# Kernel optimization log

Hardware: AMD Instinct MI355X
Metric: run time of the kernel (lower is better)

## Reference

```python
import jax, jax.numpy as jnp
import numpy as np

# Qwen3-MoE style config
B, S, D = 2, 2048, 2048        # batch, seqlen, hidden_size
E, I, TOPK = 64, 768, 8        # num_experts, moe_intermediate_size, num_experts_per_tok
M = B * S                      # tokens
CAP = 2 * (M * TOPK) // E


def setup_inputs() -> dict:
    key = jax.random.key(0)
    k0, k1, k2, k3, k4 = jax.random.split(key, 5)
    return {
        "x": jax.random.normal(k0, (B, S, D), jnp.float32),
        "router_weight": jax.random.normal(k1, (D, E), jnp.float32) * 0.02,
        "gate_proj": jax.random.normal(k2, (E, D, I), jnp.float32) * 0.02,
        "up_proj": jax.random.normal(k3, (E, D, I), jnp.float32) * 0.02,
        "down_proj": jax.random.normal(k4, (E, I, D), jnp.float32) * 0.02,
    }


def _moe(x, router_weight, gate_proj, up_proj, down_proj):
    b, s, d = x.shape
    xf = x.reshape(-1, d)                                  # [M, d]
    m = xf.shape[0]

    # ---- TokenChoiceTopKRouter: softmax scores, top-k, renormalize ----
    logits = xf @ router_weight                            # [M, E]
    probs = jax.nn.softmax(logits.astype(jnp.float32), axis=-1)
    topw, topi = jax.lax.top_k(probs, TOPK)                # [M, k]
    topw = topw / topw.sum(axis=-1, keepdims=True)         # norm_topk_prob

    flat_e = topi.reshape(-1)                              # [M*k] expert id per assignment
    flat_w = topw.reshape(-1).astype(x.dtype)              # [M*k] routing weight per assignment

    # ---- permute: sort assignments by expert (stable) ----
    order = jnp.argsort(flat_e)                            # [M*k]
    se = flat_e[order]                                     # sorted expert ids
    tok = order // TOPK                                    # source token per sorted assignment
    counts = jax.ops.segment_sum(jnp.ones_like(flat_e), flat_e, num_segments=E)
    starts = jnp.cumsum(counts) - counts                   # exclusive prefix sum
    pos = jnp.arange(m * TOPK) - starts[se]                # slot within expert's buffer
    valid = pos < CAP
    posc = jnp.minimum(pos, CAP - 1)

    # ---- dispatch to padded per-expert buffers [E, CAP, d] ----
    xe = jnp.zeros((E, CAP, d), x.dtype).at[se, pos].set(xf[tok], mode='drop')

    # ---- grouped SwiGLU experts (batched GEMMs) ----
    h = jax.nn.silu(jnp.einsum('ecd,edi->eci', xe, gate_proj)) \
        * jnp.einsum('ecd,edi->eci', xe, up_proj)          # [E, CAP, I]
    ye = jnp.einsum('eci,eid->ecd', h, down_proj)          # [E, CAP, d]

    # ---- unpermute + weighted combine ----
    contrib = jnp.where(valid[:, None], ye[se, posc], 0.0) * flat_w[order][:, None]
    out = jnp.zeros((m, d), x.dtype).at[tok].add(contrib)  # sum over topk per token
    return out.reshape(b, s, d)


def reference(x, router_weight, gate_proj, up_proj, down_proj):
    return _moe(x, router_weight, gate_proj, up_proj, down_proj)
```

## Files before the change

kernel.cpp:

```cpp
#include <hip/hip_runtime.h>
#include <hip/hip_bf16.h>

typedef __attribute__((ext_vector_type(4))) float f32x4;
typedef __attribute__((ext_vector_type(8))) short bf16x8;
typedef __attribute__((ext_vector_type(8))) unsigned short us8;
typedef unsigned int   u32;
typedef unsigned short u16;

#define D_DIM 2048
#define I_DIM 768
#define NE    64
#define CAP   1024
#define NTOK  4096

__device__ __forceinline__ u32 cvt2(float a, float b) {
  __hip_bfloat162 hh = __float22bfloat162_rn(float2{a, b});
  union { __hip_bfloat162 h; u32 u; } c; c.h = hh; return c.u;
}
__device__ __forceinline__ u16 f2b(float f) {
  __hip_bfloat16 b = __float2bfloat16(f);
  union { __hip_bfloat16 b; u16 u; } c; c.b = b; return c.u;
}
__device__ __forceinline__ float b2f(u16 v) {
  union { u32 u; float f; } c; c.u = (u32)v << 16; return c.f;
}
__device__ __forceinline__ void glp16(const void* g, void* l) {
  __builtin_amdgcn_global_load_lds(
      (const __attribute__((address_space(1))) u32*)g,
      (__attribute__((address_space(3))) u32*)l, 16, 0, 0);
}

#define VMW(n) asm volatile("s_waitcnt vmcnt(" #n ")" ::: "memory")
#define BARF   do { __builtin_amdgcn_s_barrier(); \
                    asm volatile("" ::: "memory"); } while (0)

__global__ __launch_bounds__(256) void k_router(
    const float* __restrict__ x, const float* __restrict__ rw,
    int* __restrict__ counts, int* __restrict__ slot_token,
    float* __restrict__ slot_w, u16* __restrict__ xb)
{
  const int lane = threadIdx.x & 63;
  const int tok  = blockIdx.x * 4 + (threadIdx.x >> 6);
  const float* xr = x + (size_t)tok * D_DIM;
  u16* xbr = xb + (size_t)tok * D_DIM;

  float acc = 0.f;
  for (int d0 = 0; d0 < D_DIM; d0 += 64) {
    float xv = xr[d0 + lane];
    xbr[d0 + lane] = f2b(xv);
    #pragma unroll
    for (int j = 0; j < 64; ++j) {
      float xj = __shfl(xv, j, 64);
      acc = fmaf(xj, rw[(size_t)(d0 + j) * NE + lane], acc);
    }
  }

  float v = acc; int vi = lane;
  float wk[8]; int ei[8];
  float mx0 = 0.f, wsum = 0.f;
  #pragma unroll
  for (int k = 0; k < 8; ++k) {
    float mv = v; int mi = vi;
    #pragma unroll
    for (int off = 32; off >= 1; off >>= 1) {
      float ov = __shfl_xor(mv, off, 64);
      int   oi = __shfl_xor(mi, off, 64);
      if (ov > mv || (ov == mv && oi < mi)) { mv = ov; mi = oi; }
    }
    if (k == 0) mx0 = mv;
    float ew = __expf(mv - mx0);
    wk[k] = ew; ei[k] = mi; wsum += ew;
    if (lane == mi) v = -3.4e38f;
  }

  if (lane == 0) {
    float inv = 1.f / wsum;
    #pragma unroll
    for (int k = 0; k < 8; ++k) {
      int ee   = ei[k];
      int slot = atomicAdd(&counts[ee], 1);
      if (slot < CAP) {
        slot_token[ee * CAP + slot] = tok;
        slot_w[ee * CAP + slot]     = wk[k] * inv;
      }
    }
  }
}

__global__ __launch_bounds__(256) void k_inv(
    const int* __restrict__ counts, const int* __restrict__ slot_token,
    int* __restrict__ tok_cnt, int* __restrict__ tok_idx)
{
  const int e = blockIdx.x;
  int cnt = counts[e]; if (cnt > CAP) cnt = CAP;
  for (int s = threadIdx.x; s < cnt; s += 256) {
    const int tok = slot_token[e * CAP + s];
    const int pos = atomicAdd(&tok_cnt[tok], 1);
    if (pos < 8) tok_idx[tok * 8 + pos] = e * CAP + s;
  }
}

__device__ __forceinline__ void wpack_body(const float* __restrict__ ip,
                                           u16* __restrict__ op, int R, int C,
                                           int c0, int r0) {
  __shared__ u16 T[64][76];
  const int t  = threadIdx.x;
  const int rr = t >> 4;
  const int cc = (t & 15) * 4;
  #pragma unroll
  for (int it = 0; it < 4; ++it) {
    const int r = rr + it * 16;
    float4 v = *(const float4*)(ip + (size_t)(r0 + r) * C + c0 + cc);
    T[cc + 0][r] = f2b(v.x);
    T[cc + 1][r] = f2b(v.y);
    T[cc + 2][r] = f2b(v.z);
    T[cc + 3][r] = f2b(v.w);
  }
  __syncthreads();
  const int n = t & 63;
  #pragma unroll
  for (int p = 0; p < 2; ++p) {
    const int c = (t >> 6) + p * 4;
    const u16* s = &T[n][c * 8];
    uint4 o;
    o.x = (u32)s[0] | ((u32)s[1] << 16);
    o.y = (u32)s[2] | ((u32)s[3] << 16);
    o.z = (u32)s[4] | ((u32)s[5] << 16);
    o.w = (u32)s[6] | ((u32)s[7] << 16);
    *(uint4*)(op + ((size_t)c * 64 + n) * 8) = o;
  }
}

__global__ __launch_bounds__(256) void k_wpack_gu(
    const float* __restrict__ g, const float* __restrict__ u,
    u16* __restrict__ og, u16* __restrict__ ou) {
  const int z  = blockIdx.z;
  const int e  = z >> 1;
  const float* in = (z & 1) ? u : g;
  u16* outp       = (z & 1) ? ou : og;
  const int c0 = blockIdx.x * 64;
  const int r0 = blockIdx.y * 64;
  const float* ip = in + (size_t)e * D_DIM * I_DIM;
  u16* op = outp + (size_t)e * (size_t)(I_DIM / 64) * (D_DIM / 8) * 512
                 + ((size_t)(c0 / 64) * (D_DIM / 8) + (r0 / 8)) * 512;
  wpack_body(ip, op, D_DIM, I_DIM, c0, r0);
}

__global__ __launch_bounds__(256) void k_wpack(const float* __restrict__ in,
                                               u16* __restrict__ outp,
                                               int R, int C) {
  const int e  = blockIdx.z;
  const int c0 = blockIdx.x * 64;
  const int r0 = blockIdx.y * 64;
  const float* ip = in + (size_t)e * R * C;
  u16* op = outp + (size_t)e * (size_t)(C / 64) * (R / 8) * 512
                 + ((size_t)(c0 / 64) * (R / 8) + (r0 / 8)) * 512;
  wpack_body(ip, op, R, C, c0, r0);
}

__global__ __launch_bounds__(256) void k_xpack(
    const u16* __restrict__ xb, const int* __restrict__ counts,
    const int* __restrict__ slot_token, u16* __restrict__ xeT)
{
  const int e   = blockIdx.z;
  const int s0  = blockIdx.y * 64;
  const int kc0 = blockIdx.x * 32;
  int cnt = counts[e]; if (cnt > CAP) cnt = CAP;
  const int lim = (cnt + 127) & ~127;
  if (s0 >= lim) return;

  __shared__ u16 T[64][264];
  const int t = threadIdx.x;
  const int r = t >> 2;
  const int q = t & 3;
  const int  tok  = slot_token[e * CAP + s0 + r];
  const bool live = (s0 + r) < cnt;
  const u16* src = xb + (size_t)tok * D_DIM + kc0 * 8;

  #pragma unroll
  for (int it = 0; it < 8; ++it) {
    const int kl = it * 32 + q * 8;
    us8 v = {0, 0, 0, 0, 0, 0, 0, 0};
    if (live) v = *(const us8*)(src + kl);
    *(us8*)&T[r][kl] = v;
  }
  __syncthreads();

  u16* dst = xeT + (size_t)e * 2097152 + (size_t)kc0 * 8192 + (size_t)s0 * 8;
  const int sl = t & 63;
  #pragma unroll
  for (int p = 0; p < 8; ++p) {
    const int c = (t >> 6) + p * 4;
    const u16* s = &T[sl][c * 8];
    uint4 o = *(const uint4*)s;
    *(uint4*)(dst + (size_t)c * 8192 + sl * 8) = o;
  }
}


__device__ __forceinline__ void m1_issue(
    const u16* xeA, const u16* gb, const u16* ub, u16* st,
    int js, int wv, int lane, int m0)
{
  #pragma unroll
  for (int q = 0; q < 6; ++q) {
    const int id = wv * 6 + q;
    const int kc = (id >> 1) & 3;
    const int h  = id & 1;
    const size_t kcA = (size_t)(js * 4 + kc);
    if (id < 8) {
      glp16(xeA + kcA * 8192 + (size_t)(m0 + h * 64 + lane) * 8,
            st + kc * 1024 + h * 512);
    } else if (id < 16) {
      glp16(gb + (size_t)h * 131072 + kcA * 512 + lane * 8,
            st + 4096 + kc * 1024 + h * 512);
    } else {
      glp16(ub + (size_t)h * 131072 + kcA * 512 + lane * 8,
            st + 8192 + kc * 1024 + h * 512);
    }
  }
}

__device__ __forceinline__ void m1_step(
    const u16* st, int gq, int li, int mrow, int icol,
    f32x4 (&ag)[4][4], f32x4 (&au)[4][4])
{
  bf16x8 a[4], g[4], u[4];
  #pragma unroll
  for (int mf = 0; mf < 4; ++mf)
    a[mf] = *(const bf16x8*)&st[(gq * 128 + mrow + mf * 16 + li) * 8];
  #pragma unroll
  for (int nf = 0; nf < 4; ++nf) {
    g[nf] = *(const bf16x8*)&st[4096 + (gq * 128 + icol + nf * 16 + li) * 8];
    u[nf] = *(const bf16x8*)&st[8192 + (gq * 128 + icol + nf * 16 + li) * 8];
  }
  #pragma unroll
  for (int mf = 0; mf < 4; ++mf)
    #pragma unroll
    for (int nf = 0; nf < 4; ++nf) {
      ag[mf][nf] = __builtin_amdgcn_mfma_f32_16x16x32_bf16(a[mf], g[nf], ag[mf][nf], 0, 0, 0);
      au[mf][nf] = __builtin_amdgcn_mfma_f32_16x16x32_bf16(a[mf], u[nf], au[mf][nf], 0, 0, 0);
    }
}

__global__ __launch_bounds__(256, 2) void k_mlp1p(
    const u16* __restrict__ xeT, const u16* __restrict__ Gpk,
    const u16* __restrict__ Upk, const int* __restrict__ counts,
    u16* __restrict__ hP)
{
  extern __shared__ u16 sm[];
  const int i   = blockIdx.x;
  const int xcd = i & 7;
  const int p   = i >> 3;
  const int mt  = p & 7;
  const int pe  = p >> 3;
  const int val = pe * 8 + xcd;
  const int e   = val / 6;
  const int nt  = val % 6;

  int cnt = counts[e]; if (cnt > CAP) cnt = CAP;
  const int m0 = mt * 128;
  if (m0 >= cnt) return;

  const int t = threadIdx.x;
  const int lane = t & 63, wv = t >> 6;
  const int li = lane & 15, gq = lane >> 4;
  const int mrow = (wv >> 1) * 64, icol = (wv & 1) * 64;

  const u16* xeA = xeT + (size_t)e * 2097152;
  const u16* gb  = Gpk + (size_t)e * 1572864 + (size_t)(nt * 2) * 131072;
  const u16* ub  = Upk + (size_t)e * 1572864 + (size_t)(nt * 2) * 131072;
  u16* hPe = hP + (size_t)e * 786432;

  f32x4 ag[4][4], au[4][4];
  #pragma unroll
  for (int mf = 0; mf < 4; ++mf)
    #pragma unroll
    for (int nf = 0; nf < 4; ++nf) {
      f32x4 z = {0.f, 0.f, 0.f, 0.f};
      ag[mf][nf] = z; au[mf][nf] = z;
    }

  m1_issue(xeA, gb, ub, sm,         0, wv, lane, m0);
  m1_issue(xeA, gb, ub, sm + 12288, 1, wv, lane, m0);

  for (int j = 0; j < 62; ++j) {
    VMW(6); BARF;
    m1_issue(xeA, gb, ub, sm + ((j + 2) % 3) * 12288, j + 2, wv, lane, m0);
    m1_step(sm + (j % 3) * 12288, gq, li, mrow, icol, ag, au);
  }
  VMW(6); BARF; m1_step(sm + 2 * 12288, gq, li, mrow, icol, ag, au);
  VMW(0); BARF; m1_step(sm + 0 * 12288, gq, li, mrow, icol, ag, au);

  #pragma unroll
  for (int mf = 0; mf < 4; ++mf)
    #pragma unroll
    for (int jj = 0; jj < 4; ++jj) {
      const int slot = m0 + mrow + mf * 16 + gq * 4 + jj;
      if (slot < cnt) {
        #pragma unroll
        for (int nf = 0; nf < 4; ++nf) {
          const int ii = nt * 128 + icol + nf * 16 + li;
          float gg = ag[mf][nf][jj];
          float uu = au[mf][nf][jj];
          hPe[(size_t)(ii >> 3) * 8192 + slot * 8 + (ii & 7)] =
              f2b(gg * uu / (1.f + __expf(-gg)));
        }
      }
    }
}

__device__ __forceinline__ void m2_issue(
    const u16* hPe, const u16* dp, u16* st,
    int js, int wv, int lane, int m0)
{
  #pragma unroll
  for (int q = 0; q < 6; ++q) {
    const int id = wv * 6 + q;
    const size_t kcA = (size_t)(js * 4 + ((id < 8) ? ((id >> 1) & 3) : ((id - 8) & 3)));
    if (id < 8) {
      const int kc = (id >> 1) & 3;
      const int h  = id & 1;
      glp16(hPe + kcA * 8192 + (size_t)(m0 + h * 64 + lane) * 8,
            st + kc * 1024 + h * 512);
    } else {
      const int r  = id - 8;
      const int kc = r & 3;
      const int ng = r >> 2;
      glp16(dp + (size_t)ng * 49152 + kcA * 512 + lane * 8,
            st + 4096 + kc * 2048 + ng * 512);
    }
  }
}

__device__ __forceinline__ void m2_step(
    const u16* st, int gq, int li, int mrow, int ncol,
    f32x4 (&acc)[4][8])
{
  bf16x8 a[4], b[8];
  #pragma unroll
  for (int mf = 0; mf < 4; ++mf)
    a[mf] = *(const bf16x8*)&st[(gq * 128 + mrow + mf * 16 + li) * 8];
  #pragma unroll
  for (int nf = 0; nf < 8; ++nf)
    b[nf] = *(const bf16x8*)&st[4096 + (gq * 256 + ncol + nf * 16 + li) * 8];
  #pragma unroll
  for (int mf = 0; mf < 4; ++mf)
    #pragma unroll
    for (int nf = 0; nf < 8; ++nf)
      acc[mf][nf] = __builtin_amdgcn_mfma_f32_16x16x32_bf16(a[mf], b[nf], acc[mf][nf], 0, 0, 0);
}

__global__ __launch_bounds__(256, 2) void k_mlp2p(
    const u16* __restrict__ hP, const u16* __restrict__ Dpk,
    const int* __restrict__ counts, const float* __restrict__ slot_w,
    u16* __restrict__ ye)
{
  extern __shared__ u16 sm[];
  const int i   = blockIdx.x;
  const int xcd = i & 7;
  const int p   = i >> 3;
  const int mt  = p & 7;
  const int pe  = p >> 3;
  const int val = pe * 8 + xcd;
  const int e   = val >> 3;
  const int nt  = val & 7;

  int cnt = counts[e]; if (cnt > CAP) cnt = CAP;
  const int m0 = mt * 128;
  if (m0 >= cnt) return;
  const int n0 = nt * 256;

  const int t = threadIdx.x;
  const int lane = t & 63, wv = t >> 6;
  const int li = lane & 15, gq = lane >> 4;
  const int mrow = (wv >> 1) * 64, ncol = (wv & 1) * 128;

  const u16* hPe = hP + (size_t)e * 786432;
  const u16* dp  = Dpk + (size_t)e * 1572864 + (size_t)(nt * 4) * 49152;
  const int eCAP = e * CAP;

  f32x4 acc[4][8];
  #pragma unroll
  for (int mf = 0; mf < 4; ++mf)
    #pragma unroll
    for (int nf = 0; nf < 8; ++nf) { f32x4 z = {0.f,0.f,0.f,0.f}; acc[mf][nf] = z; }

  m2_issue(hPe, dp, sm,         0, wv, lane, m0);
  m2_issue(hPe, dp, sm + 12288, 1, wv, lane, m0);

  for (int j = 0; j < 22; ++j) {
    VMW(6); BARF;
    m2_issue(hPe, dp, sm + ((j + 2) % 3) * 12288, j + 2, wv, lane, m0);
    m2_step(sm + (j % 3) * 12288, gq, li, mrow, ncol, acc);
  }
  VMW(6); BARF; m2_step(sm + (22 % 3) * 12288, gq, li, mrow, ncol, acc);
  VMW(0); BARF; m2_step(sm + (23 % 3) * 12288, gq, li, mrow, ncol, acc);

  #pragma unroll
  for (int mf = 0; mf < 4; ++mf)
    #pragma unroll
    for (int jj = 0; jj < 4; ++jj) {
      const int slot = m0 + mrow + mf * 16 + gq * 4 + jj;
      if (slot < cnt) {
        const float wgt = slot_w[eCAP + slot];
        u16* yr = ye + (size_t)(eCAP + slot) * D_DIM + n0 + ncol + li;
        #pragma unroll
        for (int nf = 0; nf < 8; ++nf)
          yr[nf * 16] = f2b(wgt * acc[mf][nf][jj]);
      }
    }
}

__global__ __launch_bounds__(256) void k_combine(
    const u16* __restrict__ ye, const int* __restrict__ tok_idx,
    const int* __restrict__ tok_cnt, float* __restrict__ out)
{
  const int tok = blockIdx.x;
  const int c0  = threadIdx.x * 8;
  int cnt8 = tok_cnt[tok]; if (cnt8 > 8) cnt8 = 8;

  float s[8] = {0.f, 0.f, 0.f, 0.f, 0.f, 0.f, 0.f, 0.f};
  #pragma unroll
  for (int k = 0; k < 8; ++k) {
    if (k < cnt8) {
      const int idx = tok_idx[tok * 8 + k];
      const us8 v = *(const us8*)(ye + (size_t)idx * D_DIM + c0);
      #pragma unroll
      for (int j = 0; j < 8; ++j) s[j] += b2f(v[j]);
    }
  }
  float4 o0 = {s[0], s[1], s[2], s[3]};
  float4 o1 = {s[4], s[5], s[6], s[7]};
  float* op = out + (size_t)tok * D_DIM + c0;
  *(float4*)op       = o0;
  *(float4*)(op + 4) = o1;
}

extern "C" void kernel_launch(void* const* d_in, const int* in_sizes, int n_in,
                              void* d_out, int out_size, void* d_ws, size_t ws_size,
                              hipStream_t stream) {
  const float* x    = (const float*)d_in[0];
  const float* rw   = (const float*)d_in[1];
  const float* gate = (const float*)d_in[2];
  const float* up   = (const float*)d_in[3];
  const float* down = (const float*)d_in[4];
  float* out = (float*)d_out;

  char* ws = (char*)d_ws;
  int*   counts     = (int*)ws;
  int*   slot_token = (int*)(ws + 1024);
  float* slot_w     = (float*)(ws + 263168);
  u16*   xb         = (u16*)(ws + 525312);
  u16*   hP         = (u16*)(ws + 17302528);
  u16*   Gpk        = (u16*)(ws + 117965824);
  u16*   Upk        = (u16*)(ws + 319292416);
  u16*   xeT        = (u16*)(ws + 520619008);
  u16*   Dpk        = xeT;
  u16*   ye         = Gpk;
  int*   tok_cnt    = (int*)(ws + 721945600);
  int*   tok_idx    = (int*)(ws + 721945600 + 16384);

  hipFuncSetAttribute((const void*)k_mlp1p,
                      hipFuncAttributeMaxDynamicSharedMemorySize, 73728);
  hipFuncSetAttribute((const void*)k_mlp2p,
                      hipFuncAttributeMaxDynamicSharedMemorySize, 73728);

  hipMemsetAsync(counts, 0, NE * sizeof(int), stream);
  hipMemsetAsync(slot_token, 0, (size_t)NE * CAP * sizeof(int), stream);

  k_router<<<dim3(NTOK / 4), 256, 0, stream>>>(x, rw, counts, slot_token, slot_w, xb);

  k_wpack_gu<<<dim3(12, 32, 2 * NE), 256, 0, stream>>>(gate, up, Gpk, Upk);
  k_xpack<<<dim3(8, 16, NE), 256, 0, stream>>>(xb, counts, slot_token, xeT);
  k_mlp1p<<<dim3(3072), 256, 73728, stream>>>(xeT, Gpk, Upk, counts, hP);

  hipMemsetAsync(tok_cnt, 0, NTOK * sizeof(int), stream);
  k_inv  <<<dim3(NE), 256, 0, stream>>>(counts, slot_token, tok_cnt, tok_idx);
  k_wpack<<<dim3(32, 12, NE), 256, 0, stream>>>(down, Dpk, I_DIM, D_DIM);

  k_mlp2p  <<<dim3(4096), 256, 73728, stream>>>(hP, Dpk, counts, slot_w, ye);
  k_combine<<<dim3(NTOK), 256, 0, stream>>>(ye, tok_idx, tok_cnt, out);
}
```

Measured before the change: 1.174 ms.

## Fuse fp32-to-bf16 weight packing into expert GEMM loads

Drops the separate weight-packing kernels and makes both expert GEMM kernels read fp32 gate/up/down weights straight from global memory into registers, convert them to bf16 and write them to LDS in the packed layout. The pipeline becomes a triple-buffered A tile fed by async loads plus a double-buffered B tile fed through registers, with a full vmcnt wait each phase. This removes a full write and re-read of packed bf16 weights, but the GEMM now moves twice the weight bytes and adds conversion work plus a stall each phase that may reduce overlap.

Measured after the change: 1.338 ms. 14.0% more time.

```diff
diff --git a/kernel.cpp b/kernel.cpp
--- a/kernel.cpp
+++ b/kernel.cpp
@@ -31,6 +31,7 @@
 }
 
 #define VMW(n) asm volatile("s_waitcnt vmcnt(" #n ")" ::: "memory")
+#define LGK    asm volatile("s_waitcnt lgkmcnt(0)" ::: "memory")
 #define BARF   do { __builtin_amdgcn_s_barrier(); \
                     asm volatile("" ::: "memory"); } while (0)
 
@@ -100,64 +101,6 @@
   }
 }
 
-__device__ __forceinline__ void wpack_body(const float* __restrict__ ip,
-                                           u16* __restrict__ op, int R, int C,
-                                           int c0, int r0) {
-  __shared__ u16 T[64][76];
-  const int t  = threadIdx.x;
-  const int rr = t >> 4;
-  const int cc = (t & 15) * 4;
-  #pragma unroll
-  for (int it = 0; it < 4; ++it) {
-    const int r = rr + it * 16;
-    float4 v = *(const float4*)(ip + (size_t)(r0 + r) * C + c0 + cc);
-    T[cc + 0][r] = f2b(v.x);
-    T[cc + 1][r] = f2b(v.y);
-    T[cc + 2][r] = f2b(v.z);
-    T[cc + 3][r] = f2b(v.w);
-  }
-  __syncthreads();
-  const int n = t & 63;
-  #pragma unroll
-  for (int p = 0; p < 2; ++p) {
-    const int c = (t >> 6) + p * 4;
-    const u16* s = &T[n][c * 8];
-    uint4 o;
-    o.x = (u32)s[0] | ((u32)s[1] << 16);
-    o.y = (u32)s[2] | ((u32)s[3] << 16);
-    o.z = (u32)s[4] | ((u32)s[5] << 16);
-    o.w = (u32)s[6] | ((u32)s[7] << 16);
-    *(uint4*)(op + ((size_t)c * 64 + n) * 8) = o;
-  }
-}
-
-__global__ __launch_bounds__(256) void k_wpack_gu(
-    const float* __restrict__ g, const float* __restrict__ u,
-    u16* __restrict__ og, u16* __restrict__ ou) {
-  const int z  = blockIdx.z;
-  const int e  = z >> 1;
-  const float* in = (z & 1) ? u : g;
-  u16* outp       = (z & 1) ? ou : og;
-  const int c0 = blockIdx.x * 64;
-  const int r0 = blockIdx.y * 64;
-  const float* ip = in + (size_t)e * D_DIM * I_DIM;
-  u16* op = outp + (size_t)e * (size_t)(I_DIM / 64) * (D_DIM / 8) * 512
-                 + ((size_t)(c0 / 64) * (D_DIM / 8) + (r0 / 8)) * 512;
-  wpack_body(ip, op, D_DIM, I_DIM, c0, r0);
-}
-
-__global__ __launch_bounds__(256) void k_wpack(const float* __restrict__ in,
-                                               u16* __restrict__ outp,
-                                               int R, int C) {
-  const int e  = blockIdx.z;
-  const int c0 = blockIdx.x * 64;
-  const int r0 = blockIdx.y * 64;
-  const float* ip = in + (size_t)e * R * C;
-  u16* op = outp + (size_t)e * (size_t)(C / 64) * (R / 8) * 512
-                 + ((size_t)(c0 / 64) * (R / 8) + (r0 / 8)) * 512;
-  wpack_body(ip, op, R, C, c0, r0);
-}
-
 __global__ __launch_bounds__(256) void k_xpack(
     const u16* __restrict__ xb, const int* __restrict__ counts,
     const int* __restrict__ slot_token, u16* __restrict__ xeT)
@@ -198,41 +141,20 @@
 }
 
 
-__device__ __forceinline__ void m1_issue(
-    const u16* xeA, const u16* gb, const u16* ub, u16* st,
-    int js, int wv, int lane, int m0)
-{
-  #pragma unroll
-  for (int q = 0; q < 6; ++q) {
-    const int id = wv * 6 + q;
-    const int kc = (id >> 1) & 3;
-    const int h  = id & 1;
-    const size_t kcA = (size_t)(js * 4 + kc);
-    if (id < 8) {
-      glp16(xeA + kcA * 8192 + (size_t)(m0 + h * 64 + lane) * 8,
-            st + kc * 1024 + h * 512);
-    } else if (id < 16) {
-      glp16(gb + (size_t)h * 131072 + kcA * 512 + lane * 8,
-            st + 4096 + kc * 1024 + h * 512);
-    } else {
-      glp16(ub + (size_t)h * 131072 + kcA * 512 + lane * 8,
-            st + 8192 + kc * 1024 + h * 512);
-    }
-  }
-}
-
 __device__ __forceinline__ void m1_step(
-    const u16* st, int gq, int li, int mrow, int icol,
+    const u16* sm, int ra, int rb, int gq, int li, int mrow, int icol,
     f32x4 (&ag)[4][4], f32x4 (&au)[4][4])
 {
+  const u16* sa = sm + ra * 4096;
+  const u16* sb = sm + 12288 + rb * 8192;
   bf16x8 a[4], g[4], u[4];
   #pragma unroll
   for (int mf = 0; mf < 4; ++mf)
-    a[mf] = *(const bf16x8*)&st[(gq * 128 + mrow + mf * 16 + li) * 8];
+    a[mf] = *(const bf16x8*)&sa[(gq * 128 + mrow + mf * 16 + li) * 8];
   #pragma unroll
   for (int nf = 0; nf < 4; ++nf) {
-    g[nf] = *(const bf16x8*)&st[4096 + (gq * 128 + icol + nf * 16 + li) * 8];
-    u[nf] = *(const bf16x8*)&st[8192 + (gq * 128 + icol + nf * 16 + li) * 8];
+    g[nf] = *(const bf16x8*)&sb[(gq * 128 + icol + nf * 16 + li) * 8];
+    u[nf] = *(const bf16x8*)&sb[4096 + (gq * 128 + icol + nf * 16 + li) * 8];
   }
   #pragma unroll
   for (int mf = 0; mf < 4; ++mf)
@@ -244,8 +166,8 @@
 }
 
 __global__ __launch_bounds__(256, 2) void k_mlp1p(
-    const u16* __restrict__ xeT, const u16* __restrict__ Gpk,
-    const u16* __restrict__ Upk, const int* __restrict__ counts,
+    const u16* __restrict__ xeT, const float* __restrict__ gate,
+    const float* __restrict__ up, const int* __restrict__ counts,
     u16* __restrict__ hP)
 {
   extern __shared__ u16 sm[];
@@ -261,16 +183,24 @@
   int cnt = counts[e]; if (cnt > CAP) cnt = CAP;
   const int m0 = mt * 128;
   if (m0 >= cnt) return;
+  const int i0 = nt * 128;
 
   const int t = threadIdx.x;
   const int lane = t & 63, wv = t >> 6;
   const int li = lane & 15, gq = lane >> 4;
   const int mrow = (wv >> 1) * 64, icol = (wv & 1) * 64;
 
-  const u16* xeA = xeT + (size_t)e * 2097152;
-  const u16* gb  = Gpk + (size_t)e * 1572864 + (size_t)(nt * 2) * 131072;
-  const u16* ub  = Upk + (size_t)e * 1572864 + (size_t)(nt * 2) * 131072;
-  u16* hPe = hP + (size_t)e * 786432;
+  const u16* ap = xeT + (size_t)e * 2097152;
+  const int a0off = (m0 + lane) * 8;
+  const int a1off = (m0 + 64 + lane) * 8;
+
+  const int tn = t >> 7;
+  const int tt = t & 127;
+  const int kg = tt >> 5;
+  const int qq = tt & 31;
+  const float* bp = (tn ? up : gate) + (size_t)e * D_DIM * I_DIM
+                    + (size_t)(kg * 8) * I_DIM + i0 + qq * 4;
+  const int bwr = 12288 + tn * 4096 + kg * 1024 + qq * 32;
 
   f32x4 ag[4][4], au[4][4];
   #pragma unroll
@@ -281,17 +211,76 @@
       ag[mf][nf] = z; au[mf][nf] = z;
     }
 
-  m1_issue(xeA, gb, ub, sm,         0, wv, lane, m0);
-  m1_issue(xeA, gb, ub, sm + 12288, 1, wv, lane, m0);
-
-  for (int j = 0; j < 62; ++j) {
-    VMW(6); BARF;
-    m1_issue(xeA, gb, ub, sm + ((j + 2) % 3) * 12288, j + 2, wv, lane, m0);
-    m1_step(sm + (j % 3) * 12288, gq, li, mrow, icol, ag, au);
-  }
-  VMW(6); BARF; m1_step(sm + 2 * 12288, gq, li, mrow, icol, ag, au);
-  VMW(0); BARF; m1_step(sm + 0 * 12288, gq, li, mrow, icol, ag, au);
-
+  float4 c0, c1, c2, c3, c4, c5, c6, c7;
+
+#define M1_ISSA(RA) do {                                          \
+    glp16(ap + (size_t)wv * 8192 + a0off, sm + (RA) * 4096 + wv * 1024);        \
+    glp16(ap + (size_t)wv * 8192 + a1off, sm + (RA) * 4096 + wv * 1024 + 512);  \
+    ap += 32768; } while (0)
+
+#define M1_ISSB() do {                                            \
+    c0 = *(const float4*)(bp);                                    \
+    c1 = *(const float4*)(bp + I_DIM);                            \
+    c2 = *(const float4*)(bp + 2 * I_DIM);                        \
+    c3 = *(const float4*)(bp + 3 * I_DIM);                        \
+    c4 = *(const float4*)(bp + 4 * I_DIM);                        \
+    c5 = *(const float4*)(bp + 5 * I_DIM);                        \
+    c6 = *(const float4*)(bp + 6 * I_DIM);                        \
+    c7 = *(const float4*)(bp + 7 * I_DIM);                        \
+    bp += 32 * I_DIM; } while (0)
+
+#define M1_WRB(RBN) do {                                          \
+    u16* d = sm + bwr + (RBN) * 8192;                             \
+    uint4 o;                                                      \
+    o.x = cvt2(c0.x, c1.x); o.y = cvt2(c2.x, c3.x);               \
+    o.z = cvt2(c4.x, c5.x); o.w = cvt2(c6.x, c7.x);               \
+    *(uint4*)(d) = o;                                             \
+    o.x = cvt2(c0.y, c1.y); o.y = cvt2(c2.y, c3.y);               \
+    o.z = cvt2(c4.y, c5.y); o.w = cvt2(c6.y, c7.y);               \
+    *(uint4*)(d + 8) = o;                                         \
+    o.x = cvt2(c0.z, c1.z); o.y = cvt2(c2.z, c3.z);               \
+    o.z = cvt2(c4.z, c5.z); o.w = cvt2(c6.z, c7.z);               \
+    *(uint4*)(d + 16) = o;                                        \
+    o.x = cvt2(c0.w, c1.w); o.y = cvt2(c2.w, c3.w);               \
+    o.z = cvt2(c4.w, c5.w); o.w = cvt2(c6.w, c7.w);               \
+    *(uint4*)(d + 24) = o; } while (0)
+
+#define M1_PH(RA, RB, RBN, RAN) do {                              \
+    M1_ISSB(); M1_ISSA(RAN);                                      \
+    m1_step(sm, RA, RB, gq, li, mrow, icol, ag, au);              \
+    VMW(0);                                                       \
+    M1_WRB(RBN);                                                  \
+    LGK; BARF; } while (0)
+
+  M1_ISSA(0); M1_ISSA(1);
+  M1_ISSB();
+  VMW(0);
+  M1_WRB(0);
+  LGK; BARF;
+
+  for (int jt = 0; jt < 10; ++jt) {
+    M1_PH(0, 0, 1, 2);
+    M1_PH(1, 1, 0, 0);
+    M1_PH(2, 0, 1, 1);
+    M1_PH(0, 1, 0, 2);
+    M1_PH(1, 0, 1, 0);
+    M1_PH(2, 1, 0, 1);
+  }
+  M1_PH(0, 0, 1, 2);
+  M1_PH(1, 1, 0, 0);
+  M1_ISSB();
+  m1_step(sm, 2, 0, gq, li, mrow, icol, ag, au);
+  VMW(0);
+  M1_WRB(1);
+  LGK; BARF;
+  m1_step(sm, 0, 1, gq, li, mrow, icol, ag, au);
+
+#undef M1_PH
+#undef M1_WRB
+#undef M1_ISSB
+#undef M1_ISSA
+
+  u16* hPe = hP + (size_t)e * 786432;
   #pragma unroll
   for (int mf = 0; mf < 4; ++mf)
     #pragma unroll
@@ -310,40 +299,19 @@
     }
 }
 
-__device__ __forceinline__ void m2_issue(
-    const u16* hPe, const u16* dp, u16* st,
-    int js, int wv, int lane, int m0)
-{
-  #pragma unroll
-  for (int q = 0; q < 6; ++q) {
-    const int id = wv * 6 + q;
-    const size_t kcA = (size_t)(js * 4 + ((id < 8) ? ((id >> 1) & 3) : ((id - 8) & 3)));
-    if (id < 8) {
-      const int kc = (id >> 1) & 3;
-      const int h  = id & 1;
-      glp16(hPe + kcA * 8192 + (size_t)(m0 + h * 64 + lane) * 8,
-            st + kc * 1024 + h * 512);
-    } else {
-      const int r  = id - 8;
-      const int kc = r & 3;
-      const int ng = r >> 2;
-      glp16(dp + (size_t)ng * 49152 + kcA * 512 + lane * 8,
-            st + 4096 + kc * 2048 + ng * 512);
-    }
-  }
-}
-
 __device__ __forceinline__ void m2_step(
-    const u16* st, int gq, int li, int mrow, int ncol,
+    const u16* sm, int ra, int rb, int gq, int li, int mrow, int ncol,
     f32x4 (&acc)[4][8])
 {
+  const u16* sa = sm + ra * 4096;
+  const u16* sb = sm + 12288 + rb * 8192;
   bf16x8 a[4], b[8];
   #pragma unroll
   for (int mf = 0; mf < 4; ++mf)
-    a[mf] = *(const bf16x8*)&st[(gq * 128 + mrow + mf * 16 + li) * 8];
+    a[mf] = *(const bf16x8*)&sa[(gq * 128 + mrow + mf * 16 + li) * 8];
   #pragma unroll
   for (int nf = 0; nf < 8; ++nf)
-    b[nf] = *(const bf16x8*)&st[4096 + (gq * 256 + ncol + nf * 16 + li) * 8];
+    b[nf] = *(const bf16x8*)&sb[(gq * 256 + ncol + nf * 16 + li) * 8];
   #pragma unroll
   for (int mf = 0; mf < 4; ++mf)
     #pragma unroll
@@ -352,7 +320,7 @@
 }
 
 __global__ __launch_bounds__(256, 2) void k_mlp2p(
-    const u16* __restrict__ hP, const u16* __restrict__ Dpk,
+    const u16* __restrict__ hP, const float* __restrict__ down,
     const int* __restrict__ counts, const float* __restrict__ slot_w,
     u16* __restrict__ ye)
 {
@@ -376,8 +344,16 @@
   const int li = lane & 15, gq = lane >> 4;
   const int mrow = (wv >> 1) * 64, ncol = (wv & 1) * 128;
 
-  const u16* hPe = hP + (size_t)e * 786432;
-  const u16* dp  = Dpk + (size_t)e * 1572864 + (size_t)(nt * 4) * 49152;
+  const u16* ap = hP + (size_t)e * 786432;
+  const int a0off = (m0 + lane) * 8;
+  const int a1off = (m0 + 64 + lane) * 8;
+
+  const int kg = t >> 6;
+  const int qq = t & 63;
+  const float* bp = down + (size_t)e * I_DIM * D_DIM
+                    + (size_t)(kg * 8) * D_DIM + n0 + qq * 4;
+  const int bwr = 12288 + kg * 2048 + qq * 32;
+
   const int eCAP = e * CAP;
 
   f32x4 acc[4][8];
@@ -386,16 +362,76 @@
     #pragma unroll
     for (int nf = 0; nf < 8; ++nf) { f32x4 z = {0.f,0.f,0.f,0.f}; acc[mf][nf] = z; }
 
-  m2_issue(hPe, dp, sm,         0, wv, lane, m0);
-  m2_issue(hPe, dp, sm + 12288, 1, wv, lane, m0);
-
-  for (int j = 0; j < 22; ++j) {
-    VMW(6); BARF;
-    m2_issue(hPe, dp, sm + ((j + 2) % 3) * 12288, j + 2, wv, lane, m0);
-    m2_step(sm + (j % 3) * 12288, gq, li, mrow, ncol, acc);
-  }
-  VMW(6); BARF; m2_step(sm + (22 % 3) * 12288, gq, li, mrow, ncol, acc);
-  VMW(0); BARF; m2_step(sm + (23 % 3) * 12288, gq, li, mrow, ncol, acc);
+  float4 c0, c1, c2, c3, c4, c5, c6, c7;
+
+#define M2_ISSA(RA) do {                                          \
+    glp16(ap + (size_t)wv * 8192 + a0off, sm + (RA) * 4096 + wv * 1024);        \
+    glp16(ap + (size_t)wv * 8192 + a1off, sm + (RA) * 4096 + wv * 1024 + 512);  \
+    ap += 32768; } while (0)
+
+#define M2_ISSB() do {                                            \
+    c0 = *(const float4*)(bp);                                    \
+    c1 = *(const float4*)(bp + D_DIM);                            \
+    c2 = *(const float4*)(bp + 2 * D_DIM);                        \
+    c3 = *(const float4*)(bp + 3 * D_DIM);                        \
+    c4 = *(const float4*)(bp + 4 * D_DIM);                        \
+    c5 = *(const float4*)(bp + 5 * D_DIM);                        \
+    c6 = *(const float4*)(bp + 6 * D_DIM);                        \
+    c7 = *(const float4*)(bp + 7 * D_DIM);                        \
+    bp += 32 * D_DIM; } while (0)
+
+#define M2_WRB(RBN) do {                                          \
+    u16* d = sm + bwr + (RBN) * 8192;                             \
+    uint4 o;                                                      \
+    o.x = cvt2(c0.x, c1.x); o.y = cvt2(c2.x, c3.x);               \
+    o.z = cvt2(c4.x, c5.x); o.w = cvt2(c6.x, c7.x);               \
+    *(uint4*)(d) = o;                                             \
+    o.x = cvt2(c0.y, c1.y); o.y = cvt2(c2.y, c3.y);               \
+    o.z = cvt2(c4.y, c5.y); o.w = cvt2(c6.y, c7.y);               \
+    *(uint4*)(d + 8) = o;                                         \
+    o.x = cvt2(c0.z, c1.z); o.y = cvt2(c2.z, c3.z);               \
+    o.z = cvt2(c4.z, c5.z); o.w = cvt2(c6.z, c7.z);               \
+    *(uint4*)(d + 16) = o;                                        \
+    o.x = cvt2(c0.w, c1.w); o.y = cvt2(c2.w, c3.w);               \
+    o.z = cvt2(c4.w, c5.w); o.w = cvt2(c6.w, c7.w);               \
+    *(uint4*)(d + 24) = o; } while (0)
+
+#define M2_PH(RA, RB, RBN, RAN) do {                              \
+    M2_ISSB(); M2_ISSA(RAN);                                      \
+    m2_step(sm, RA, RB, gq, li, mrow, ncol, acc);                 \
+    VMW(0);                                                       \
+    M2_WRB(RBN);                                                  \
+    LGK; BARF; } while (0)
+
+  M2_ISSA(0); M2_ISSA(1);
+  M2_ISSB();
+  VMW(0);
+  M2_WRB(0);
+  LGK; BARF;
+
+  for (int jt = 0; jt < 3; ++jt) {
+    M2_PH(0, 0, 1, 2);
+    M2_PH(1, 1, 0, 0);
+    M2_PH(2, 0, 1, 1);
+    M2_PH(0, 1, 0, 2);
+    M2_PH(1, 0, 1, 0);
+    M2_PH(2, 1, 0, 1);
+  }
+  M2_PH(0, 0, 1, 2);
+  M2_PH(1, 1, 0, 0);
+  M2_PH(2, 0, 1, 1);
+  M2_PH(0, 1, 0, 2);
+  M2_ISSB();
+  m2_step(sm, 1, 0, gq, li, mrow, ncol, acc);
+  VMW(0);
+  M2_WRB(1);
+  LGK; BARF;
+  m2_step(sm, 2, 1, gq, li, mrow, ncol, acc);
+
+#undef M2_PH
+#undef M2_WRB
+#undef M2_ISSB
+#undef M2_ISSA
 
   #pragma unroll
   for (int mf = 0; mf < 4; ++mf)
@@ -453,32 +489,26 @@
   float* slot_w     = (float*)(ws + 263168);
   u16*   xb         = (u16*)(ws + 525312);
   u16*   hP         = (u16*)(ws + 17302528);
-  u16*   Gpk        = (u16*)(ws + 117965824);
-  u16*   Upk        = (u16*)(ws + 319292416);
+  u16*   ye         = (u16*)(ws + 117965824);
   u16*   xeT        = (u16*)(ws + 520619008);
-  u16*   Dpk        = xeT;
-  u16*   ye         = Gpk;
   int*   tok_cnt    = (int*)(ws + 721945600);
   int*   tok_idx    = (int*)(ws + 721945600 + 16384);
 
   hipFuncSetAttribute((const void*)k_mlp1p,
-                      hipFuncAttributeMaxDynamicSharedMemorySize, 73728);
+                      hipFuncAttributeMaxDynamicSharedMemorySize, 57344);
   hipFuncSetAttribute((const void*)k_mlp2p,
-                      hipFuncAttributeMaxDynamicSharedMemorySize, 73728);
+                      hipFuncAttributeMaxDynamicSharedMemorySize, 57344);
 
   hipMemsetAsync(counts, 0, NE * sizeof(int), stream);
   hipMemsetAsync(slot_token, 0, (size_t)NE * CAP * sizeof(int), stream);
 
   k_router<<<dim3(NTOK / 4), 256, 0, stream>>>(x, rw, counts, slot_token, slot_w, xb);
-
-  k_wpack_gu<<<dim3(12, 32, 2 * NE), 256, 0, stream>>>(gate, up, Gpk, Upk);
   k_xpack<<<dim3(8, 16, NE), 256, 0, stream>>>(xb, counts, slot_token, xeT);
-  k_mlp1p<<<dim3(3072), 256, 73728, stream>>>(xeT, Gpk, Upk, counts, hP);
+  k_mlp1p<<<dim3(3072), 256, 57344, stream>>>(xeT, gate, up, counts, hP);
 
   hipMemsetAsync(tok_cnt, 0, NTOK * sizeof(int), stream);
-  k_inv  <<<dim3(NE), 256, 0, stream>>>(counts, slot_token, tok_cnt, tok_idx);
-  k_wpack<<<dim3(32, 12, NE), 256, 0, stream>>>(down, Dpk, I_DIM, D_DIM);
-
-  k_mlp2p  <<<dim3(4096), 256, 73728, stream>>>(hP, Dpk, counts, slot_w, ye);
+  k_inv<<<dim3(NE), 256, 0, stream>>>(counts, slot_token, tok_cnt, tok_idx);
+
+  k_mlp2p  <<<dim3(4096), 256, 57344, stream>>>(hP, down, counts, slot_w, ye);
   k_combine<<<dim3(NTOK), 256, 0, stream>>>(ye, tok_idx, tok_cnt, out);
 }
```
